# Kernel tuning notes

Measured on AMD Instinct MI355X. Metric: run time of the kernel, lower is better.

The kernel has to match this reference:

```python
import jax, jax.numpy as jnp
import numpy as np

B, S, D, H = 2, 2048, 1024, 16
DK = D // H


def setup_inputs() -> dict:
    key = jax.random.key(0)
    ks = jax.random.split(key, 12)
    std = 1.0 / np.sqrt(D)
    inp = {
        "query": jax.random.normal(ks[0], (B, S, D), jnp.float32),
        "key": jax.random.normal(ks[1], (B, S, D), jnp.float32),
        "value": jax.random.normal(ks[2], (B, S, D), jnp.float32),
        # causal mask: 1 = keep, 0 = blocked (matches masked_fill(mask==0, -inf))
        "mask": jnp.tril(jnp.ones((S, S), jnp.int32))[None, None, :, :],
        # torch Linear convention: W is (out, in), y = x @ W.T + b
        "Wq": jax.random.normal(ks[3], (D, D), jnp.float32) * std,
        "bq": jax.random.normal(ks[4], (D,), jnp.float32) * std,
        "Wk": jax.random.normal(ks[5], (D, D), jnp.float32) * std,
        "bk": jax.random.normal(ks[6], (D,), jnp.float32) * std,
        "Wv": jax.random.normal(ks[7], (D, D), jnp.float32) * std,
        "bv": jax.random.normal(ks[8], (D,), jnp.float32) * std,
        "Wo": jax.random.normal(ks[9], (D, D), jnp.float32) * std,
        "bo": jax.random.normal(ks[10], (D,), jnp.float32) * std,
    }
    return inp


def reference(query, key, value, mask, Wq, bq, Wk, bk, Wv, bv, Wo, bo):
    b = query.shape[0]
    # projections (torch Linear: x @ W.T + b)
    Q = query @ Wq.T + bq
    K = key @ Wk.T + bk
    V = value @ Wv.T + bv
    # (b, s, d) -> (b, h, s, dk)
    Q = Q.reshape(b, -1, H, DK).transpose(0, 2, 1, 3)
    K = K.reshape(b, -1, H, DK).transpose(0, 2, 1, 3)
    V = V.reshape(b, -1, H, DK).transpose(0, 2, 1, 3)
    scores = jnp.einsum("bhqd,bhkd->bhqk", Q, K) / jnp.sqrt(jnp.float32(DK))
    scores = jnp.where(mask == 0, -jnp.inf, scores)
    weights = jax.nn.softmax(scores, axis=-1)  # dropout p=0.0 / eval mode: no-op
    attn = jnp.einsum("bhqk,bhkd->bhqd", weights, V)
    attn = attn.transpose(0, 2, 1, 3).reshape(b, -1, D)
    return attn @ Wo.T + bo
```

## Files before the change

### kernel.cpp

```cpp
#include <hip/hip_runtime.h>
#include <hip/hip_bf16.h>
#include <cstdint>
#include <cstddef>


#define B_ 2
#define S_ 2048
#define D_ 1024
#define H_ 16
#define DK_ 64
#define QSCALE 0.1803368801111244f

typedef __attribute__((ext_vector_type(8))) short bf16x8;
typedef __attribute__((ext_vector_type(4))) float f32x4;
typedef __attribute__((ext_vector_type(16))) float f32x16;
typedef __attribute__((ext_vector_type(4))) unsigned short u16x4;
typedef __attribute__((ext_vector_type(4))) float float4v;
typedef __attribute__((ext_vector_type(2))) unsigned int u32x2;
typedef __attribute__((ext_vector_type(4))) unsigned int u32x4;

__device__ __forceinline__ unsigned short f2bf(float f) {
  unsigned int u = __float_as_uint(f);
  u += 0x7FFFu + ((u >> 16) & 1u);
  return (unsigned short)(u >> 16);
}
__device__ __forceinline__ unsigned int cvt_pk_bf16(float lo, float hi) {
  unsigned int r;
  asm("v_cvt_pk_bf16_f32 %0, %1, %2" : "=v"(r) : "v"(lo), "v"(hi));
  return r;
}
__device__ __forceinline__ bf16x8 lds_read_sw64(const unsigned short* base, int row, int col) {
  int P = (row * 64 + col) * 2;
  int X = P ^ ((row & 7) << 4);
  return *(const bf16x8*)((const char*)base + X);
}

__global__ __launch_bounds__(256) void cvt3(const float* __restrict__ s0,
                                            const float* __restrict__ s1,
                                            const float* __restrict__ s2,
                                            unsigned short* __restrict__ d0,
                                            unsigned short* __restrict__ d1,
                                            unsigned short* __restrict__ d2) {
  const float* src = blockIdx.y == 0 ? s0 : blockIdx.y == 1 ? s1 : s2;
  unsigned short* dst = blockIdx.y == 0 ? d0 : blockIdx.y == 1 ? d1 : d2;
  int i = blockIdx.x * 256 + threadIdx.x;
  float4v v = *(const float4v*)(src + (size_t)i * 4);
  u16x4 o;
  o[0] = f2bf(v[0]); o[1] = f2bf(v[1]); o[2] = f2bf(v[2]); o[3] = f2bf(v[3]);
  *(u16x4*)(dst + (size_t)i * 4) = o;
}

__global__ __launch_bounds__(256) void cvt4(const float* __restrict__ s0,
                                            const float* __restrict__ s1,
                                            const float* __restrict__ s2,
                                            const float* __restrict__ s3,
                                            unsigned short* __restrict__ d0,
                                            unsigned short* __restrict__ d1,
                                            unsigned short* __restrict__ d2,
                                            unsigned short* __restrict__ d3) {
  int z = blockIdx.y;
  const float* src = z == 0 ? s0 : z == 1 ? s1 : z == 2 ? s2 : s3;
  unsigned short* dst = z == 0 ? d0 : z == 1 ? d1 : z == 2 ? d2 : d3;
  int i = blockIdx.x * 256 + threadIdx.x;
  float4v v = *(const float4v*)(src + (size_t)i * 4);
  u16x4 o;
  o[0] = f2bf(v[0]); o[1] = f2bf(v[1]); o[2] = f2bf(v[2]); o[3] = f2bf(v[3]);
  *(u16x4*)(dst + (size_t)i * 4) = o;
}

__global__ __launch_bounds__(256) void gemm_qkv(
    const unsigned short* __restrict__ Xq, const unsigned short* __restrict__ Xk,
    const unsigned short* __restrict__ Xv, const unsigned short* __restrict__ Wq,
    const unsigned short* __restrict__ Wk, const unsigned short* __restrict__ Wv,
    const float* __restrict__ bq, const float* __restrict__ bk,
    const float* __restrict__ bv, unsigned short* __restrict__ Qp,
    unsigned short* __restrict__ Kp, unsigned short* __restrict__ Vt) {
  const int z = blockIdx.z;
  const unsigned short* A = z == 0 ? Xq : z == 1 ? Xk : Xv;
  const unsigned short* W = z == 0 ? Wq : z == 1 ? Wk : Wv;
  const float* bias = z == 0 ? bq : z == 1 ? bk : bv;
  const int K = D_, N = D_;

  __shared__ __align__(16) unsigned short As[128 * 64];
  __shared__ __align__(16) unsigned short Bs[128 * 64];
  const int tid  = threadIdx.x;
  const int lane = tid & 63;
  const int m0 = blockIdx.x * 128;
  const int n0 = blockIdx.y * 128;
  const int wr = ((tid >> 6) >> 1) * 64;
  const int wc = ((tid >> 6) & 1) * 64;
  const int lr = lane & 15;
  const int lk = (lane >> 4) * 8;
  f32x4 acc[4][4] = {};

  int dstX[4], srow[4], scolu[4];
#pragma unroll
  for (int i = 0; i < 4; ++i) {
    int X = tid * 16 + i * 4096;
    int P = X ^ (((X >> 7) & 7) << 4);
    dstX[i] = X;
    srow[i] = P >> 7;
    scolu[i] = (P & 127) >> 1;
  }

  for (int k0 = 0; k0 < K; k0 += 64) {
    __syncthreads();
#pragma unroll
    for (int i = 0; i < 4; ++i) {
      const unsigned short* gA = A + (size_t)(m0 + srow[i]) * K + k0 + scolu[i];
      const unsigned short* gB = W + (size_t)(n0 + srow[i]) * K + k0 + scolu[i];
      __builtin_amdgcn_global_load_lds((const __attribute__((address_space(1))) void*)gA,
          (__attribute__((address_space(3))) void*)((char*)As + dstX[i]), 16, 0, 0);
      __builtin_amdgcn_global_load_lds((const __attribute__((address_space(1))) void*)gB,
          (__attribute__((address_space(3))) void*)((char*)Bs + dstX[i]), 16, 0, 0);
    }
    __syncthreads();
#pragma unroll
    for (int kk = 0; kk < 2; ++kk) {
      bf16x8 a[4], b[4];
#pragma unroll
      for (int m = 0; m < 4; ++m)
        a[m] = lds_read_sw64(As, wr + m * 16 + lr, kk * 32 + lk);
#pragma unroll
      for (int n = 0; n < 4; ++n)
        b[n] = lds_read_sw64(Bs, wc + n * 16 + lr, kk * 32 + lk);
#pragma unroll
      for (int m = 0; m < 4; ++m)
#pragma unroll
        for (int n = 0; n < 4; ++n)
          acc[m][n] = __builtin_amdgcn_mfma_f32_16x16x32_bf16(a[m], b[n], acc[m][n], 0, 0, 0);
    }
  }

  const int rbase = (lane >> 4) * 4;
  if (z == 2) {
#pragma unroll
    for (int m = 0; m < 4; ++m)
#pragma unroll
      for (int n = 0; n < 4; ++n) {
        int col = n0 + wc + n * 16 + lr;
        float bvv = bias[col];
        int row0 = m0 + wr + m * 16 + rbase;
        int bb = row0 >> 11, s = row0 & 2047;
        int h = col >> 6, dk = col & 63;
        u16x4 o;
#pragma unroll
        for (int r = 0; r < 4; ++r) o[r] = f2bf(acc[m][n][r] + bvv);
        size_t idx = (((size_t)bb * H_ + h) * DK_ + dk) * S_ + s;
        *(u16x4*)(Vt + idx) = o;
      }
  } else {
    unsigned short* Cout = z == 0 ? Qp : Kp;
    const float scale = z == 0 ? QSCALE : 1.0f;
#pragma unroll
    for (int m = 0; m < 4; ++m)
#pragma unroll
      for (int n = 0; n < 4; ++n) {
        int col = n0 + wc + n * 16 + lr;
        float bvv = bias[col];
#pragma unroll
        for (int r = 0; r < 4; ++r) {
          int row = m0 + wr + m * 16 + rbase + r;
          Cout[(size_t)row * N + col] = f2bf((acc[m][n][r] + bvv) * scale);
        }
      }
  }
}

__global__ __launch_bounds__(256) void gemm_o(const unsigned short* __restrict__ A,
                                              const unsigned short* __restrict__ W,
                                              const float* __restrict__ bias,
                                              float* __restrict__ C,
                                              int M, int N, int K) {
  __shared__ __align__(16) unsigned short As[64 * 64];
  __shared__ __align__(16) unsigned short Bs[128 * 64];
  const int tid  = threadIdx.x;
  const int lane = tid & 63;
  const int m0 = blockIdx.x * 64;
  const int n0 = blockIdx.y * 128;
  const int wr = ((tid >> 6) >> 1) * 32;
  const int wc = ((tid >> 6) & 1) * 64;
  const int lr = lane & 15;
  const int lk = (lane >> 4) * 8;
  f32x4 acc[2][4] = {};

  int dstX[4], srow[4], scolu[4];
#pragma unroll
  for (int i = 0; i < 4; ++i) {
    int X = tid * 16 + i * 4096;
    int P = X ^ (((X >> 7) & 7) << 4);
    dstX[i] = X;
    srow[i] = P >> 7;
    scolu[i] = (P & 127) >> 1;
  }

  for (int k0 = 0; k0 < K; k0 += 64) {
    __syncthreads();
#pragma unroll
    for (int i = 0; i < 2; ++i) {
      const unsigned short* gA = A + (size_t)(m0 + srow[i]) * K + k0 + scolu[i];
      __builtin_amdgcn_global_load_lds((const __attribute__((address_space(1))) void*)gA,
          (__attribute__((address_space(3))) void*)((char*)As + dstX[i]), 16, 0, 0);
    }
#pragma unroll
    for (int i = 0; i < 4; ++i) {
      const unsigned short* gB = W + (size_t)(n0 + srow[i]) * K + k0 + scolu[i];
      __builtin_amdgcn_global_load_lds((const __attribute__((address_space(1))) void*)gB,
          (__attribute__((address_space(3))) void*)((char*)Bs + dstX[i]), 16, 0, 0);
    }
    __syncthreads();
#pragma unroll
    for (int kk = 0; kk < 2; ++kk) {
      bf16x8 a[2], b[4];
#pragma unroll
      for (int m = 0; m < 2; ++m)
        a[m] = lds_read_sw64(As, wr + m * 16 + lr, kk * 32 + lk);
#pragma unroll
      for (int n = 0; n < 4; ++n)
        b[n] = lds_read_sw64(Bs, wc + n * 16 + lr, kk * 32 + lk);
#pragma unroll
      for (int m = 0; m < 2; ++m)
#pragma unroll
        for (int n = 0; n < 4; ++n)
          acc[m][n] = __builtin_amdgcn_mfma_f32_16x16x32_bf16(a[m], b[n], acc[m][n], 0, 0, 0);
    }
  }

  const int rbase = (lane >> 4) * 4;
#pragma unroll
  for (int m = 0; m < 2; ++m)
#pragma unroll
    for (int n = 0; n < 4; ++n) {
      int col = n0 + wc + n * 16 + lr;
      float bvv = bias[col];
#pragma unroll
      for (int r = 0; r < 4; ++r) {
        int row = m0 + wr + m * 16 + rbase + r;
        C[(size_t)row * N + col] = acc[m][n][r] + bvv;
      }
    }
}

__device__ __forceinline__ bf16x8 lds_read_swK(const unsigned short* base, int row, int col) {
  int P = (row * 64 + col) * 2;
  int X = P ^ ((row & 7) << 4);
  return *(const bf16x8*)((const char*)base + X);
}
__device__ __forceinline__ bf16x8 lds_read_swV(const unsigned short* base, int row, int col) {
  int P = (row * 128 + col) * 2;
  int X = P ^ ((row & 7) << 4);
  return *(const bf16x8*)((const char*)base + X);
}

__global__ __launch_bounds__(256) void flash_attn(const unsigned short* __restrict__ Qp,
                                                  const unsigned short* __restrict__ Kp,
                                                  const unsigned short* __restrict__ Vtp,
                                                  unsigned short* __restrict__ Op) {
  __shared__ __align__(16) unsigned short smem[32768];

  const int tid  = threadIdx.x;
  const int lane = tid & 63;
  const int w = tid >> 6;
  const int qh = w & 1;
  const int kp = w >> 1;
  const int h  = blockIdx.y;
  const int b  = blockIdx.z;
  const int ql = lane & 31;
  const int hi5 = lane >> 5;
  const size_t basebs = (size_t)b * S_ * D_;
  const int hoff = h * DK_;

  const unsigned short* gK0 = Kp + basebs + hoff;
  const unsigned short* gV0 = Vtp + ((size_t)b * H_ + h) * DK_ * S_;

  int dstXK[4], srcK[4], srcV[4];
#pragma unroll
  for (int i = 0; i < 4; ++i) {
    int X = tid * 16 + i * 4096;
    int Pk = X ^ (((X >> 7) & 7) << 4);
    dstXK[i] = X;
    srcK[i] = (Pk >> 7) * D_ + ((Pk & 127) >> 1);
    int Pv = X ^ (((X >> 8) & 7) << 4);
    srcV[i] = (Pv >> 8) * S_ + ((Pv & 255) >> 1);
  }

#define STAGE(RR, BUF)                                                         \
  {                                                                            \
    const unsigned short* gK = gK0 + (size_t)((RR) * 128) * D_;                \
    const unsigned short* gV = gV0 + (RR) * 128;                               \
    char* kb = (char*)smem + (BUF) * 32768;                                    \
    char* vb = kb + 16384;                                                     \
    _Pragma("unroll")                                                          \
    for (int i = 0; i < 4; ++i) {                                              \
      __builtin_amdgcn_global_load_lds(                                        \
          (const __attribute__((address_space(1))) void*)(gK + srcK[i]),       \
          (__attribute__((address_space(3))) void*)(kb + dstXK[i]), 16, 0, 0); \
      __builtin_amdgcn_global_load_lds(                                        \
          (const __attribute__((address_space(1))) void*)(gV + srcV[i]),       \
          (__attribute__((address_space(3))) void*)(vb + dstXK[i]), 16, 0, 0); \
    }                                                                          \
  }

  for (int s = 0; s < 2; ++s) {
    const int qt = s == 0 ? 31 - (int)blockIdx.x : (int)blockIdx.x;
    const int q0 = qt * 64;
    const int qbase = q0 + qh * 32;
    const int qglob = qbase + ql;

    bf16x8 qf[4];
    {
      const unsigned short* qrow = Qp + basebs + (size_t)qglob * D_ + hoff;
#pragma unroll
      for (int f = 0; f < 4; ++f)
        qf[f] = *(const bf16x8*)(qrow + f * 16 + hi5 * 8);
    }

    float m_r = -1e30f;
    float l_r = 0.f;
    f32x16 out0 = {};
    f32x16 out1 = {};

    const int R = (qt + 2) >> 1;

    STAGE(0, 0);
    __syncthreads();

    for (int r = 0; r < R; ++r) {
      const int cur = r & 1;
      if (r + 1 < R) STAGE(r + 1, cur ^ 1);

      const unsigned short* Kb = smem + cur * 16384;
      const unsigned short* Vb = Kb + 8192;

      const int kv0w = r * 128 + kp * 64;
      const bool do0 = (kv0w <= qbase);
      const bool do1 = (kv0w + 32 <= qbase);
      const bool part0 = (kv0w == qbase);
      const bool part1 = (kv0w + 32 == qbase);

      if (do0) {
        f32x16 sc0 = {}, sc1 = {};
        __builtin_amdgcn_s_setprio(1);
#pragma unroll
        for (int f = 0; f < 4; ++f) {
          bf16x8 kf = lds_read_swK(Kb, kp * 64 + ql, f * 16 + hi5 * 8);
          sc0 = __builtin_amdgcn_mfma_f32_32x32x16_bf16(kf, qf[f], sc0, 0, 0, 0);
        }
        if (do1) {
#pragma unroll
          for (int f = 0; f < 4; ++f) {
            bf16x8 kf = lds_read_swK(Kb, kp * 64 + 32 + ql, f * 16 + hi5 * 8);
            sc1 = __builtin_amdgcn_mfma_f32_32x32x16_bf16(kf, qf[f], sc1, 0, 0, 0);
          }
        }
        __builtin_amdgcn_s_setprio(0);

        if (part0) {
#pragma unroll
          for (int g = 0; g < 16; ++g) {
            int kvg = kv0w + (g & 3) + 8 * (g >> 2) + 4 * hi5;
            if (kvg > qglob) sc0[g] = -1e30f;
          }
        }
        if (do1 && part1) {
#pragma unroll
          for (int g = 0; g < 16; ++g) {
            int kvg = kv0w + 32 + (g & 3) + 8 * (g >> 2) + 4 * hi5;
            if (kvg > qglob) sc1[g] = -1e30f;
          }
        }

        float pm = sc0[0];
#pragma unroll
        for (int g = 1; g < 16; ++g) pm = fmaxf(pm, sc0[g]);
        if (do1) {
#pragma unroll
          for (int g = 0; g < 16; ++g) pm = fmaxf(pm, sc1[g]);
        }
        pm = fmaxf(pm, __shfl_xor(pm, 32));

        if (!__all(pm - m_r <= 8.0f)) {
          float mnew = fmaxf(m_r, pm);
          float scl = __builtin_exp2f(m_r - mnew);
          l_r *= scl;
#pragma unroll
          for (int g = 0; g < 16; ++g) { out0[g] *= scl; out1[g] *= scl; }
          m_r = mnew;
        }

        float l_add = 0.f;
#define PV_CHUNK(SVEC, HALF, C)                                                \
        {                                                                      \
          const int g0 = (HALF) * 8;                                           \
          float p0 = __builtin_exp2f((SVEC)[g0 + 0] - m_r);                    \
          float p1 = __builtin_exp2f((SVEC)[g0 + 1] - m_r);                    \
          float p2 = __builtin_exp2f((SVEC)[g0 + 2] - m_r);                    \
          float p3 = __builtin_exp2f((SVEC)[g0 + 3] - m_r);                    \
          float p4 = __builtin_exp2f((SVEC)[g0 + 4] - m_r);                    \
          float p5 = __builtin_exp2f((SVEC)[g0 + 5] - m_r);                    \
          float p6 = __builtin_exp2f((SVEC)[g0 + 6] - m_r);                    \
          float p7 = __builtin_exp2f((SVEC)[g0 + 7] - m_r);                    \
          l_add += ((p0 + p1) + (p2 + p3)) + ((p4 + p5) + (p6 + p7));          \
          unsigned int u0 = cvt_pk_bf16(p0, p1);                               \
          unsigned int u1 = cvt_pk_bf16(p2, p3);                               \
          unsigned int u2 = cvt_pk_bf16(p4, p5);                               \
          unsigned int u3 = cvt_pk_bf16(p6, p7);                               \
          unsigned int ta = hi5 ? u0 : u2, tb = hi5 ? u1 : u3;                 \
          unsigned int ra = (unsigned int)__shfl_xor((int)ta, 32);             \
          unsigned int rb = (unsigned int)__shfl_xor((int)tb, 32);             \
          u32x4 pw = {hi5 ? ra : u0, hi5 ? rb : u1,                            \
                      hi5 ? u2 : ra, hi5 ? u3 : rb};                           \
          bf16x8 pf = __builtin_bit_cast(bf16x8, pw);                          \
          bf16x8 vf0 = lds_read_swV(Vb, ql, kp * 64 + (C) * 16 + hi5 * 8);     \
          out0 = __builtin_amdgcn_mfma_f32_32x32x16_bf16(vf0, pf, out0, 0, 0, 0);\
          bf16x8 vf1 = lds_read_swV(Vb, 32 + ql, kp * 64 + (C) * 16 + hi5 * 8);\
          out1 = __builtin_amdgcn_mfma_f32_32x32x16_bf16(vf1, pf, out1, 0, 0, 0);\
        }
        __builtin_amdgcn_s_setprio(1);
        PV_CHUNK(sc0, 0, 0);
        PV_CHUNK(sc0, 1, 1);
        if (do1) {
          PV_CHUNK(sc1, 0, 2);
          PV_CHUNK(sc1, 1, 3);
        }
        __builtin_amdgcn_s_setprio(0);
#undef PV_CHUNK

        l_add += __shfl_xor(l_add, 32);
        l_r += l_add;
      }
      __syncthreads();
    }

    float* scr = (float*)smem;
    if (kp == 1) {
      float* p = scr + ((size_t)qh * 64 + lane) * 34;
#pragma unroll
      for (int g = 0; g < 16; ++g) { p[g] = out0[g]; p[16 + g] = out1[g]; }
      p[32] = m_r;
      p[33] = l_r;
    }
    __syncthreads();
    if (kp == 0) {
      const float* p = scr + ((size_t)qh * 64 + lane) * 34;
      float m1 = p[32], l1 = p[33];
      float mM = fmaxf(m_r, m1);
      float s0 = __builtin_exp2f(m_r - mM);
      float s1 = __builtin_exp2f(m1 - mM);
      float rcp = 1.0f / (l_r * s0 + l1 * s1);
      float a0 = s0 * rcp, a1 = s1 * rcp;
      unsigned short* orow = Op + basebs + (size_t)qglob * D_ + hoff;
#pragma unroll
      for (int i = 0; i < 4; ++i) {
        u32x2 o0 = {cvt_pk_bf16(out0[4 * i + 0] * a0 + p[4 * i + 0] * a1,
                                out0[4 * i + 1] * a0 + p[4 * i + 1] * a1),
                    cvt_pk_bf16(out0[4 * i + 2] * a0 + p[4 * i + 2] * a1,
                                out0[4 * i + 3] * a0 + p[4 * i + 3] * a1)};
        *(u32x2*)(orow + 8 * i + 4 * hi5) = o0;
        u32x2 o1 = {cvt_pk_bf16(out1[4 * i + 0] * a0 + p[16 + 4 * i + 0] * a1,
                                out1[4 * i + 1] * a0 + p[16 + 4 * i + 1] * a1),
                    cvt_pk_bf16(out1[4 * i + 2] * a0 + p[16 + 4 * i + 2] * a1,
                                out1[4 * i + 3] * a0 + p[16 + 4 * i + 3] * a1)};
        *(u32x2*)(orow + 32 + 8 * i + 4 * hi5) = o1;
      }
    }
    __syncthreads();
  }
#undef STAGE
}

extern "C" void kernel_launch(void* const* d_in, const int* in_sizes, int n_in,
                              void* d_out, int out_size, void* d_ws, size_t ws_size,
                              hipStream_t stream) {
  const float* q  = (const float*)d_in[0];
  const float* k  = (const float*)d_in[1];
  const float* v  = (const float*)d_in[2];
  const float* Wq = (const float*)d_in[4];
  const float* bq = (const float*)d_in[5];
  const float* Wk = (const float*)d_in[6];
  const float* bk = (const float*)d_in[7];
  const float* Wv = (const float*)d_in[8];
  const float* bv = (const float*)d_in[9];
  const float* Wo = (const float*)d_in[10];
  const float* bo = (const float*)d_in[11];

  const int MSD = B_ * S_;
  unsigned short* ws = (unsigned short*)d_ws;
  unsigned short* Xq  = ws;
  unsigned short* Xk  = Xq  + (size_t)MSD * D_;
  unsigned short* Xv  = Xk  + (size_t)MSD * D_;
  unsigned short* Wqb = Xv  + (size_t)MSD * D_;
  unsigned short* Wkb = Wqb + (size_t)D_ * D_;
  unsigned short* Wvb = Wkb + (size_t)D_ * D_;
  unsigned short* Wob = Wvb + (size_t)D_ * D_;
  unsigned short* Qp  = Wob + (size_t)D_ * D_;
  unsigned short* Kp  = Qp  + (size_t)MSD * D_;
  unsigned short* Vt  = Kp  + (size_t)MSD * D_;
  unsigned short* At  = Vt  + (size_t)MSD * D_;

  const int n4a = MSD * D_ / 4;
  const int n4w = D_ * D_ / 4;
  dim3 g3(n4a / 256, 3);
  cvt3<<<g3, 256, 0, stream>>>(q, k, v, Xq, Xk, Xv);
  dim3 g4(n4w / 256, 4);
  cvt4<<<g4, 256, 0, stream>>>(Wq, Wk, Wv, Wo, Wqb, Wkb, Wvb, Wob);

  dim3 gqkv(MSD / 128, D_ / 128, 3);
  gemm_qkv<<<gqkv, 256, 0, stream>>>(Xq, Xk, Xv, Wqb, Wkb, Wvb,
                                     bq, bk, bv, Qp, Kp, Vt);

  dim3 ga(16, H_, B_);
  flash_attn<<<ga, 256, 0, stream>>>(Qp, Kp, Vt, At);

  dim3 go(MSD / 64, D_ / 128);
  gemm_o<<<go, 256, 0, stream>>>(At, Wob, bo, (float*)d_out, MSD, D_, D_);
}
```

Before: 131.3 us.

## Split flash attention KV tile across four wave pairs with 512-thread blocks

The attention block grows from 4 to 8 waves. Each KV tile of 128 keys is now split four ways, so each wave pair handles 32 keys instead of 64, with a three-way merge of partial softmax state at the end. The goal is more parallel waves per tile and a shorter per-wave dependency chain, which should hide latency better. The cost is more register pressure under the launch bounds, more scratch traffic and merge work in the epilogue, and partial results that are more often idle on causal tiles.

Result: no change. 133.2 us (+1.5%).

```diff
diff --git a/kernel.cpp b/kernel.cpp
--- a/kernel.cpp
+++ b/kernel.cpp
@@ -252,17 +252,17 @@
   return *(const bf16x8*)((const char*)base + X);
 }
 
-__global__ __launch_bounds__(256) void flash_attn(const unsigned short* __restrict__ Qp,
-                                                  const unsigned short* __restrict__ Kp,
-                                                  const unsigned short* __restrict__ Vtp,
-                                                  unsigned short* __restrict__ Op) {
+__global__ __launch_bounds__(512, 4) void flash_attn(const unsigned short* __restrict__ Qp,
+                                                     const unsigned short* __restrict__ Kp,
+                                                     const unsigned short* __restrict__ Vtp,
+                                                     unsigned short* __restrict__ Op) {
   __shared__ __align__(16) unsigned short smem[32768];
 
   const int tid  = threadIdx.x;
   const int lane = tid & 63;
   const int w = tid >> 6;
   const int qh = w & 1;
-  const int kp = w >> 1;
+  const int kq = w >> 1;
   const int h  = blockIdx.y;
   const int b  = blockIdx.z;
   const int ql = lane & 31;
@@ -273,10 +273,10 @@
   const unsigned short* gK0 = Kp + basebs + hoff;
   const unsigned short* gV0 = Vtp + ((size_t)b * H_ + h) * DK_ * S_;
 
-  int dstXK[4], srcK[4], srcV[4];
-#pragma unroll
-  for (int i = 0; i < 4; ++i) {
-    int X = tid * 16 + i * 4096;
+  int dstXK[2], srcK[2], srcV[2];
+#pragma unroll
+  for (int i = 0; i < 2; ++i) {
+    int X = tid * 16 + i * 8192;
     int Pk = X ^ (((X >> 7) & 7) << 4);
     dstXK[i] = X;
     srcK[i] = (Pk >> 7) * D_ + ((Pk & 127) >> 1);
@@ -291,7 +291,7 @@
     char* kb = (char*)smem + (BUF) * 32768;                                    \
     char* vb = kb + 16384;                                                     \
     _Pragma("unroll")                                                          \
-    for (int i = 0; i < 4; ++i) {                                              \
+    for (int i = 0; i < 2; ++i) {                                              \
       __builtin_amdgcn_global_load_lds(                                        \
           (const __attribute__((address_space(1))) void*)(gK + srcK[i]),       \
           (__attribute__((address_space(3))) void*)(kb + dstXK[i]), 16, 0, 0); \
@@ -332,51 +332,31 @@
       const unsigned short* Kb = smem + cur * 16384;
       const unsigned short* Vb = Kb + 8192;
 
-      const int kv0w = r * 128 + kp * 64;
-      const bool do0 = (kv0w <= qbase);
-      const bool do1 = (kv0w + 32 <= qbase);
-      const bool part0 = (kv0w == qbase);
-      const bool part1 = (kv0w + 32 == qbase);
-
-      if (do0) {
-        f32x16 sc0 = {}, sc1 = {};
+      const int kv0w = r * 128 + kq * 32;
+      const bool act = (kv0w <= qbase);
+      const bool part = (kv0w == qbase);
+
+      if (act) {
+        f32x16 sc = {};
         __builtin_amdgcn_s_setprio(1);
 #pragma unroll
         for (int f = 0; f < 4; ++f) {
-          bf16x8 kf = lds_read_swK(Kb, kp * 64 + ql, f * 16 + hi5 * 8);
-          sc0 = __builtin_amdgcn_mfma_f32_32x32x16_bf16(kf, qf[f], sc0, 0, 0, 0);
+          bf16x8 kf = lds_read_swK(Kb, kq * 32 + ql, f * 16 + hi5 * 8);
+          sc = __builtin_amdgcn_mfma_f32_32x32x16_bf16(kf, qf[f], sc, 0, 0, 0);
         }
-        if (do1) {
-#pragma unroll
-          for (int f = 0; f < 4; ++f) {
-            bf16x8 kf = lds_read_swK(Kb, kp * 64 + 32 + ql, f * 16 + hi5 * 8);
-            sc1 = __builtin_amdgcn_mfma_f32_32x32x16_bf16(kf, qf[f], sc1, 0, 0, 0);
+        __builtin_amdgcn_s_setprio(0);
+
+        if (part) {
+#pragma unroll
+          for (int g = 0; g < 16; ++g) {
+            int kvg = kv0w + (g & 3) + 8 * (g >> 2) + 4 * hi5;
+            if (kvg > qglob) sc[g] = -1e30f;
           }
         }
-        __builtin_amdgcn_s_setprio(0);
-
-        if (part0) {
-#pragma unroll
-          for (int g = 0; g < 16; ++g) {
-            int kvg = kv0w + (g & 3) + 8 * (g >> 2) + 4 * hi5;
-            if (kvg > qglob) sc0[g] = -1e30f;
-          }
-        }
-        if (do1 && part1) {
-#pragma unroll
-          for (int g = 0; g < 16; ++g) {
-            int kvg = kv0w + 32 + (g & 3) + 8 * (g >> 2) + 4 * hi5;
-            if (kvg > qglob) sc1[g] = -1e30f;
-          }
-        }
-
-        float pm = sc0[0];
-#pragma unroll
-        for (int g = 1; g < 16; ++g) pm = fmaxf(pm, sc0[g]);
-        if (do1) {
-#pragma unroll
-          for (int g = 0; g < 16; ++g) pm = fmaxf(pm, sc1[g]);
-        }
+
+        float pm = sc[0];
+#pragma unroll
+        for (int g = 1; g < 16; ++g) pm = fmaxf(pm, sc[g]);
         pm = fmaxf(pm, __shfl_xor(pm, 32));
 
         if (!__all(pm - m_r <= 8.0f)) {
@@ -389,17 +369,17 @@
         }
 
         float l_add = 0.f;
-#define PV_CHUNK(SVEC, HALF, C)                                                \
+#define PV_CHUNK(HALF)                                                         \
         {                                                                      \
           const int g0 = (HALF) * 8;                                           \
-          float p0 = __builtin_exp2f((SVEC)[g0 + 0] - m_r);                    \
-          float p1 = __builtin_exp2f((SVEC)[g0 + 1] - m_r);                    \
-          float p2 = __builtin_exp2f((SVEC)[g0 + 2] - m_r);                    \
-          float p3 = __builtin_exp2f((SVEC)[g0 + 3] - m_r);                    \
-          float p4 = __builtin_exp2f((SVEC)[g0 + 4] - m_r);                    \
-          float p5 = __builtin_exp2f((SVEC)[g0 + 5] - m_r);                    \
-          float p6 = __builtin_exp2f((SVEC)[g0 + 6] - m_r);                    \
-          float p7 = __builtin_exp2f((SVEC)[g0 + 7] - m_r);                    \
+          float p0 = __builtin_exp2f(sc[g0 + 0] - m_r);                        \
+          float p1 = __builtin_exp2f(sc[g0 + 1] - m_r);                        \
+          float p2 = __builtin_exp2f(sc[g0 + 2] - m_r);                        \
+          float p3 = __builtin_exp2f(sc[g0 + 3] - m_r);                        \
+          float p4 = __builtin_exp2f(sc[g0 + 4] - m_r);                        \
+          float p5 = __builtin_exp2f(sc[g0 + 5] - m_r);                        \
+          float p6 = __builtin_exp2f(sc[g0 + 6] - m_r);                        \
+          float p7 = __builtin_exp2f(sc[g0 + 7] - m_r);                        \
           l_add += ((p0 + p1) + (p2 + p3)) + ((p4 + p5) + (p6 + p7));          \
           unsigned int u0 = cvt_pk_bf16(p0, p1);                               \
           unsigned int u1 = cvt_pk_bf16(p2, p3);                               \
@@ -411,18 +391,15 @@
           u32x4 pw = {hi5 ? ra : u0, hi5 ? rb : u1,                            \
                       hi5 ? u2 : ra, hi5 ? u3 : rb};                           \
           bf16x8 pf = __builtin_bit_cast(bf16x8, pw);                          \
-          bf16x8 vf0 = lds_read_swV(Vb, ql, kp * 64 + (C) * 16 + hi5 * 8);     \
+          int vcol = kq * 32 + (HALF) * 16 + hi5 * 8;                          \
+          bf16x8 vf0 = lds_read_swV(Vb, ql, vcol);                             \
           out0 = __builtin_amdgcn_mfma_f32_32x32x16_bf16(vf0, pf, out0, 0, 0, 0);\
-          bf16x8 vf1 = lds_read_swV(Vb, 32 + ql, kp * 64 + (C) * 16 + hi5 * 8);\
+          bf16x8 vf1 = lds_read_swV(Vb, 32 + ql, vcol);                       \
           out1 = __builtin_amdgcn_mfma_f32_32x32x16_bf16(vf1, pf, out1, 0, 0, 0);\
         }
         __builtin_amdgcn_s_setprio(1);
-        PV_CHUNK(sc0, 0, 0);
-        PV_CHUNK(sc0, 1, 1);
-        if (do1) {
-          PV_CHUNK(sc1, 0, 2);
-          PV_CHUNK(sc1, 1, 3);
-        }
+        PV_CHUNK(0);
+        PV_CHUNK(1);
         __builtin_amdgcn_s_setprio(0);
 #undef PV_CHUNK
 
@@ -433,34 +410,40 @@
     }
 
     float* scr = (float*)smem;
-    if (kp == 1) {
-      float* p = scr + ((size_t)qh * 64 + lane) * 34;
+    if (kq != 0) {
+      float* p = scr + (((size_t)qh * 3 + (kq - 1)) * 64 + lane) * 34;
 #pragma unroll
       for (int g = 0; g < 16; ++g) { p[g] = out0[g]; p[16 + g] = out1[g]; }
       p[32] = m_r;
       p[33] = l_r;
     }
     __syncthreads();
-    if (kp == 0) {
-      const float* p = scr + ((size_t)qh * 64 + lane) * 34;
-      float m1 = p[32], l1 = p[33];
-      float mM = fmaxf(m_r, m1);
-      float s0 = __builtin_exp2f(m_r - mM);
-      float s1 = __builtin_exp2f(m1 - mM);
-      float rcp = 1.0f / (l_r * s0 + l1 * s1);
-      float a0 = s0 * rcp, a1 = s1 * rcp;
+    if (kq == 0) {
+      float mA = m_r, lA = l_r;
+#pragma unroll
+      for (int j = 0; j < 3; ++j) {
+        const float* p = scr + (((size_t)qh * 3 + j) * 64 + lane) * 34;
+        float mj = p[32], lj = p[33];
+        float mM = fmaxf(mA, mj);
+        float s0 = __builtin_exp2f(mA - mM);
+        float s1 = __builtin_exp2f(mj - mM);
+#pragma unroll
+        for (int g = 0; g < 16; ++g) {
+          out0[g] = out0[g] * s0 + p[g] * s1;
+          out1[g] = out1[g] * s0 + p[16 + g] * s1;
+        }
+        lA = lA * s0 + lj * s1;
+        mA = mM;
+      }
+      float rcp = 1.0f / lA;
       unsigned short* orow = Op + basebs + (size_t)qglob * D_ + hoff;
 #pragma unroll
       for (int i = 0; i < 4; ++i) {
-        u32x2 o0 = {cvt_pk_bf16(out0[4 * i + 0] * a0 + p[4 * i + 0] * a1,
-                                out0[4 * i + 1] * a0 + p[4 * i + 1] * a1),
-                    cvt_pk_bf16(out0[4 * i + 2] * a0 + p[4 * i + 2] * a1,
-                                out0[4 * i + 3] * a0 + p[4 * i + 3] * a1)};
+        u32x2 o0 = {cvt_pk_bf16(out0[4 * i + 0] * rcp, out0[4 * i + 1] * rcp),
+                    cvt_pk_bf16(out0[4 * i + 2] * rcp, out0[4 * i + 3] * rcp)};
         *(u32x2*)(orow + 8 * i + 4 * hi5) = o0;
-        u32x2 o1 = {cvt_pk_bf16(out1[4 * i + 0] * a0 + p[16 + 4 * i + 0] * a1,
-                                out1[4 * i + 1] * a0 + p[16 + 4 * i + 1] * a1),
-                    cvt_pk_bf16(out1[4 * i + 2] * a0 + p[16 + 4 * i + 2] * a1,
-                                out1[4 * i + 3] * a0 + p[16 + 4 * i + 3] * a1)};
+        u32x2 o1 = {cvt_pk_bf16(out1[4 * i + 0] * rcp, out1[4 * i + 1] * rcp),
+                    cvt_pk_bf16(out1[4 * i + 2] * rcp, out1[4 * i + 3] * rcp)};
         *(u32x2*)(orow + 32 + 8 * i + 4 * hi5) = o1;
       }
     }
@@ -510,7 +493,7 @@
                                      bq, bk, bv, Qp, Kp, Vt);
 
   dim3 ga(16, H_, B_);
-  flash_attn<<<ga, 256, 0, stream>>>(Qp, Kp, Vt, At);
+  flash_attn<<<ga, 512, 0, stream>>>(Qp, Kp, Vt, At);
 
   dim3 go(MSD / 64, D_ / 128);
   gemm_o<<<go, 256, 0, stream>>>(At, Wob, bo, (float*)d_out, MSD, D_, D_);
```
